# Performance work log

Hardware: AMD Instinct MI355X
Metric: run time of the kernel (lower is better)

Reference implementation:

```python
import jax, jax.numpy as jnp
import numpy as np

B, T_ENC, T_DEC = 1024, 96, 16
P_Q, CFG, H = 235, 32, 256
D_IN = P_Q + 5 + 10 + 3 + 3  # 256, matches input_size in __init__


def _lstm_step(x, h, c, Wih, Whh, bih, bhh):
    # torch.nn.LSTMCell: gate order i, f, g, o
    g = x @ Wih.T + bih + h @ Whh.T + bhh
    i, f, gg, o = jnp.split(g, 4, axis=-1)
    c2 = jax.nn.sigmoid(f) * c + jax.nn.sigmoid(i) * jnp.tanh(gg)
    h2 = jax.nn.sigmoid(o) * jnp.tanh(c2)
    return h2, c2


def setup_inputs():
    key = jax.random.key(0)
    ks = jax.random.split(key, 30)
    s = 0.05

    def n(i, shape):
        return jax.random.normal(ks[i], shape, jnp.float32) * s

    return {
        "input_p_q": jax.random.normal(ks[0], (B, T_ENC, P_Q), jnp.float32),
        "input_config": jax.random.normal(ks[1], (B, T_ENC, CFG), jnp.float32),
        "input_time": jax.random.randint(ks[2], (B, T_ENC, 3), 0, 5, jnp.int32),
        "W_cfg": n(3, (10, CFG)), "b_cfg": n(4, (10,)),
        "E_hour": n(5, (24, 5)), "E_wd": n(6, (8, 3)), "E_season": n(7, (5, 3)),
        "Wih_e": n(8, (4 * H, D_IN)), "Whh_e": n(9, (4 * H, H)),
        "bih_e": n(10, (4 * H,)), "bhh_e": n(11, (4 * H,)),
        "Wih_d": n(12, (4, H + 1)), "Whh_d": n(13, (4, 1)),
        "bih_d": n(14, (4,)), "bhh_d": n(15, (4,)),
        "Wi_s": n(16, (H, D_IN)), "bi_s": n(17, (H,)),
        "We_s": n(18, (H, 2 * H)),
        "Vd_s": n(19, (1, H)), "bVd_s": n(20, (1,)),
        "Wd_t": n(21, (H, H)), "bd_t": n(22, (H,)),
        "Wd2_t": n(23, (H, 2)),
        "Vd_t": n(24, (1, H)), "bVd_t": n(25, (1,)),
    }


def _forward(input_p_q, input_config, input_time, W_cfg, b_cfg, E_hour, E_wd, E_season,
             Wih_e, Whh_e, bih_e, bhh_e, Wih_d, Whh_d, bih_d, bhh_d,
             Wi_s, bi_s, We_s, Vd_s, bVd_s, Wd_t, bd_t, Wd2_t, Vd_t, bVd_t):
    b = input_p_q.shape[0]
    cfg = input_config @ W_cfg.T + b_cfg  # [B,T,10]
    inputs = jnp.concatenate([
        input_p_q, cfg,
        E_hour[input_time[:, :, 0]],
        E_wd[input_time[:, :, 1]],
        E_season[input_time[:, :, 2]],
    ], axis=2)  # [B,T,D_IN]

    # spatial_attention_Wi(inputs) hoisted out of the per-step loop (identical math)
    wi = inputs @ Wi_s.T + bi_s  # [B,T,H]

    def enc_step(carry, xt):
        hi, ci = carry
        x_t, wi_t = xt
        # Vd(tanh(We([h,c]) + Wi(x)))  -> [B,1] scalar gate (no softmax in original)
        a = jnp.tanh(jnp.concatenate([hi, ci], axis=1) @ We_s.T + wi_t) @ Vd_s.T + bVd_s
        h2, c2 = _lstm_step(x_t * a, hi, ci, Wih_e, Whh_e, bih_e, bhh_e)
        return (h2, c2), h2

    h0 = jnp.zeros((b, H), inputs.dtype)
    (_, _), mid = jax.lax.scan(enc_step, (h0, h0),
                               (inputs.transpose(1, 0, 2), wi.transpose(1, 0, 2)))
    mid = mid.transpose(1, 0, 2)  # [B,T,H]

    # temporal_attention_Wd(mid) does not depend on decode step -> hoisted
    wd_mid = mid @ Wd_t.T + bd_t  # [B,T,H]
    prev0 = mid[:, -1, 2:3]       # [B,1], as in original (element 2 of last hidden)

    def dec_step(carry, _):
        hi, ci, prev = carry
        q = jnp.concatenate([hi, ci], axis=1) @ Wd2_t.T       # [B,H]
        a = jnp.tanh(q[:, None, :] + wd_mid) @ Vd_t.T + bVd_t  # [B,T,1], raw scores
        ctx = jnp.einsum('bth,bt->bh', mid, a[..., 0])          # weighted sum over T
        h2, c2 = _lstm_step(jnp.concatenate([ctx, prev], axis=1), hi, ci,
                            Wih_d, Whh_d, bih_d, bhh_d)
        return (h2, c2, h2), h2

    z = jnp.zeros((b, 1), inputs.dtype)
    _, dec = jax.lax.scan(dec_step, (z, z, prev0), None, length=T_DEC)
    return dec.transpose(1, 0, 2)  # [B,16,1]


def reference(input_p_q, input_config, input_time, W_cfg, b_cfg, E_hour, E_wd, E_season,
              Wih_e, Whh_e, bih_e, bhh_e, Wih_d, Whh_d, bih_d, bhh_d,
              Wi_s, bi_s, We_s, Vd_s, bVd_s, Wd_t, bd_t, Wd2_t, Vd_t, bVd_t):
    return _forward(input_p_q, input_config, input_time, W_cfg, b_cfg, E_hour, E_wd,
                    E_season, Wih_e, Whh_e, bih_e, bhh_e, Wih_d, Whh_d, bih_d, bhh_d,
                    Wi_s, bi_s, We_s, Vd_s, bVd_s, Wd_t, bd_t, Wd2_t, Vd_t, bVd_t)
```

## Files before the change

### kernel.cpp

```cpp
#include <hip/hip_runtime.h>
#include <hip/hip_bf16.h>


typedef unsigned short ushort_t;
using short4v = __attribute__((ext_vector_type(4))) short;
using short8  = __attribute__((ext_vector_type(8))) short;
using floatx4 = __attribute__((ext_vector_type(4))) float;

#define DEVFN static __device__ __forceinline__

DEVFN float bs2f(ushort_t u) {
    union { float f; unsigned v; } c; c.v = ((unsigned)u) << 16; return c.f;
}
DEVFN ushort_t f2bs(float f) {
    __hip_bfloat16 h = __float2bfloat16(f);
    return *reinterpret_cast<ushort_t*>(&h);
}
DEVFN float gload(const void* p, long i, int bf) {
    if (bf) return bs2f(((const ushort_t*)p)[i]);
    return ((const float*)p)[i];
}
DEVFN float sigm(float x) { return 1.f / (1.f + __expf(-x)); }
DEVFN float ftanh(float x) {
    float t = __expf(-2.f * fabsf(x));
    float r = (1.f - t) / (1.f + t);
    return copysignf(r, x);
}
DEVFN short8 ld8(const ushort_t* p) { return *reinterpret_cast<const short8*>(p); }

DEVFN void bar_lgkm() {
    asm volatile("s_waitcnt lgkmcnt(0)" ::: "memory");
    __builtin_amdgcn_s_barrier();
}

#define GLD16R(dst, src) \
    asm volatile("global_load_dwordx4 %0, %1, off" : "+v"(dst) : "v"(src))

#define VW3() do { asm volatile("s_waitcnt vmcnt(3)"); \
                   __builtin_amdgcn_sched_barrier(0x3F7); } while (0)

struct SrcPtrs { const void* p[26]; };
struct WsPtrs {
    ushort_t *wcfg, *bcfg, *eh, *ew, *es, *wis, *bis, *wes, *vds, *bvds,
             *whh, *wih, *bih, *bhh, *wdt, *bdt, *wd2t, *vdt, *bvdt,
             *wihd, *whhd, *bihd, *bhhd;
};

__global__ void k_detect(const void* probe, int* flag) {
    if (threadIdx.x == 0 && blockIdx.x == 0) {
        const ushort_t* u = (const ushort_t*)probe;
        int ok = 1;
        for (int i = 0; i < 16; ++i) {
            ushort_t v = u[2 * i];
            int e = (v >> 7) & 0xFF;
            if (!(v == 0 || (e >= 96 && e <= 126))) ok = 0;
        }
        *flag = ok;
    }
}

__global__ __launch_bounds__(256) void k_cvt(SrcPtrs sp, WsPtrs wp, const int* flagp) {
    int bf = *flagp;
    const void* src = nullptr; ushort_t* dst = nullptr; long n = 0;
    switch (blockIdx.x) {
        case 0:  src = sp.p[3];  dst = wp.wcfg; n = 320;    break;
        case 1:  src = sp.p[4];  dst = wp.bcfg; n = 10;     break;
        case 2:  src = sp.p[5];  dst = wp.eh;   n = 120;    break;
        case 3:  src = sp.p[6];  dst = wp.ew;   n = 24;     break;
        case 4:  src = sp.p[7];  dst = wp.es;   n = 15;     break;
        case 5:  src = sp.p[16]; dst = wp.wis;  n = 65536;  break;
        case 6:  src = sp.p[17]; dst = wp.bis;  n = 256;    break;
        case 8:  src = sp.p[19]; dst = wp.vds;  n = 256;    break;
        case 9:  src = sp.p[20]; dst = wp.bvds; n = 1;      break;
        case 12: src = sp.p[10]; dst = wp.bih;  n = 1024;   break;
        case 13: src = sp.p[11]; dst = wp.bhh;  n = 1024;   break;
        case 14: src = sp.p[21]; dst = wp.wdt;  n = 65536;  break;
        case 15: src = sp.p[22]; dst = wp.bdt;  n = 256;    break;
        case 16: src = sp.p[23]; dst = wp.wd2t; n = 512;    break;
        case 17: src = sp.p[24]; dst = wp.vdt;  n = 256;    break;
        case 18: src = sp.p[25]; dst = wp.bvdt; n = 1;      break;
        case 19: src = sp.p[12]; dst = wp.wihd; n = 1028;   break;
        case 20: src = sp.p[13]; dst = wp.whhd; n = 4;      break;
        case 21: src = sp.p[14]; dst = wp.bihd; n = 4;      break;
        case 22: src = sp.p[15]; dst = wp.bhhd; n = 4;      break;
        default: return;
    }
    for (long i = threadIdx.x; i < n; i += 256) {
        float v = bf ? bs2f(((const ushort_t*)src)[i]) : ((const float*)src)[i];
        dst[i] = f2bs(v);
    }
}

__global__ __launch_bounds__(256) void k_permA(
    const void* whh_src, const void* wih_src,
    ushort_t* whhp, ushort_t* wihb, const int* flagp)
{
    int bf = *flagp;
    long base = (long)blockIdx.x * 2048;
    if (blockIdx.y == 1) {
#pragma unroll
        for (int ii = 0; ii < 8; ++ii) {
            long p = base + threadIdx.x + ii * 256;
            wihb[p] = f2bs(gload(wih_src, p, bf));
        }
        return;
    }
#pragma unroll
    for (int ii = 0; ii < 8; ++ii) {
        long p = base + threadIdx.x + ii * 256;
        int c = (int)(p >> 9), l = (int)((p >> 3) & 63), e = (int)(p & 7);
        int w = c >> 5, kk = (c >> 2) & 7, g = c & 3;
        int q = l >> 4, ln = l & 15;
        long si = (long)(g * 256 + w * 16 + ln) * 256 + kk * 32 + q * 8 + e;
        whhp[p] = f2bs(gload(whh_src, si, bf));
    }
}

__global__ __launch_bounds__(256) void k_permB(
    const void* wes_src, ushort_t* wesp, const int* flagp)
{
    int bf = *flagp;
    long base = (long)blockIdx.x * 2048;
#pragma unroll
    for (int ii = 0; ii < 8; ++ii) {
        long p = base + threadIdx.x + ii * 256;
        int c = (int)(p >> 9), l = (int)((p >> 3) & 63), e = (int)(p & 7);
        int w = c >> 4, kk = c & 15;
        int q = l >> 4, ln = l & 15;
        long si = (long)(w * 16 + ln) * 512 + kk * 32 + q * 8 + e;
        wesp[p] = f2bs(gload(wes_src, si, bf));
    }
}

__global__ __launch_bounds__(256) void k_build(
    const void* __restrict__ pq, const void* __restrict__ cfg_in,
    const int* __restrict__ timei, WsPtrs wp, const int* __restrict__ flagp,
    ushort_t* __restrict__ inputs)
{
    int bf = *flagp;
    int ch = threadIdx.x;
    for (int rr = 0; rr < 4; ++rr) {
        long row = (long)blockIdx.x * 4 + rr;
        float v;
        if (ch < 235) {
            v = gload(pq, row * 235 + ch, bf);
        } else if (ch < 245) {
            int j = ch - 235;
            float acc = bs2f(wp.bcfg[j]);
            for (int k = 0; k < 32; ++k)
                acc += gload(cfg_in, row * 32 + k, bf) * bs2f(wp.wcfg[j * 32 + k]);
            v = acc;
        } else if (ch < 250) {
            v = bs2f(wp.eh[timei[row * 3 + 0] * 5 + (ch - 245)]);
        } else if (ch < 253) {
            v = bs2f(wp.ew[timei[row * 3 + 1] * 3 + (ch - 250)]);
        } else {
            v = bs2f(wp.es[timei[row * 3 + 2] * 3 + (ch - 253)]);
        }
        inputs[row * 256 + ch] = f2bs(v);
    }
}

__global__ __launch_bounds__(256) void k_gemm(
    const ushort_t* __restrict__ A, const ushort_t* __restrict__ W,
    const ushort_t* __restrict__ bias, ushort_t* __restrict__ out,
    int ostride, int gatherB)
{
    const int K = 256;
    __shared__ alignas(16) ushort_t At[128][40];
    __shared__ alignas(16) ushort_t Bt[128][40];

    int tid  = threadIdx.x;
    int lane = tid & 63, wave = tid >> 6;
    int wm = wave >> 1, wn = wave & 1;
    int q = lane >> 4, ln = lane & 15;
    long mbase = (long)blockIdx.x * 128;

    floatx4 acc[4][4];
#pragma unroll
    for (int i = 0; i < 4; ++i)
#pragma unroll
        for (int j = 0; j < 4; ++j) acc[i][j] = (floatx4){0.f, 0.f, 0.f, 0.f};

    for (int k0 = 0; k0 < K; k0 += 32) {
        __syncthreads();
#pragma unroll
        for (int it = 0; it < 2; ++it) {
            int c = tid + it * 256;
            int r = c >> 2, kc = (c & 3) * 8;
            int wrow = gatherB ? (((r & 3) << 8) + ((int)blockIdx.y << 5) + (r >> 2))
                               : ((int)blockIdx.y * 128 + r);
            *reinterpret_cast<short8*>(&At[r][kc]) = ld8(&A[(mbase + r) * K + k0 + kc]);
            *reinterpret_cast<short8*>(&Bt[r][kc]) = ld8(&W[(long)wrow * K + k0 + kc]);
        }
        __syncthreads();
        short8 af[4];
#pragma unroll
        for (int mt = 0; mt < 4; ++mt)
            af[mt] = *reinterpret_cast<const short8*>(&At[wm * 64 + mt * 16 + ln][q * 8]);
#pragma unroll
        for (int nt = 0; nt < 4; ++nt) {
            short8 bf = *reinterpret_cast<const short8*>(&Bt[wn * 64 + nt * 16 + ln][q * 8]);
#pragma unroll
            for (int mt = 0; mt < 4; ++mt)
                acc[mt][nt] = __builtin_amdgcn_mfma_f32_16x16x32_bf16(af[mt], bf, acc[mt][nt], 0, 0, 0);
        }
    }

#pragma unroll
    for (int mt = 0; mt < 4; ++mt)
#pragma unroll
        for (int nt = 0; nt < 4; ++nt)
#pragma unroll
            for (int reg = 0; reg < 4; ++reg) {
                long row = mbase + wm * 64 + mt * 16 + q * 4 + reg;
                int  col = (int)blockIdx.y * 128 + wn * 64 + nt * 16 + ln;
                float bv = bias ? bs2f(bias[col]) : 0.f;
                out[row * (long)ostride + col] = f2bs(acc[mt][nt][reg] + bv);
            }
}

#define MFMA16(a, b, c) __builtin_amdgcn_mfma_f32_16x16x32_bf16((a), (b), (c), 0, 0, 0)

__global__ __launch_bounds__(512) void k_encoder(
    const ushort_t* __restrict__ wi, const ushort_t* __restrict__ ax,
    WsPtrs wp, ushort_t* __restrict__ mid)
{
    __shared__ alignas(16) ushort_t hcb[2][16][520];
    __shared__ alignas(16) float aPartT[16][20];
    __shared__ ushort_t occupancy_pad[30720];

    int tid  = threadIdx.x;
    int lane = tid & 63, w = tid >> 6;
    int q = lane >> 4, ln = lane & 15;
    long row0 = (long)blockIdx.x * 16;
    int u0 = w * 32 + ln;

    for (int i = tid; i < 2 * 16 * 520; i += 512) ((ushort_t*)hcb)[i] = 0;

    float bc[2][4], vds[2];
#pragma unroll
    for (int s = 0; s < 2; ++s) {
        int us = u0 + s * 16;
        bc[s][0] = bs2f(wp.bih[us])       + bs2f(wp.bhh[us]);
        bc[s][1] = bs2f(wp.bih[256 + us]) + bs2f(wp.bhh[256 + us]);
        bc[s][2] = bs2f(wp.bih[512 + us]) + bs2f(wp.bhh[512 + us]);
        bc[s][3] = bs2f(wp.bih[768 + us]) + bs2f(wp.bhh[768 + us]);
        vds[s]   = bs2f(wp.vds[us]);
    }
    float bVd = bs2f(wp.bvds[0]);

    const ushort_t* wesW0 = wp.wes + ((long)(2 * w)     << 13) + lane * 8;
    const ushort_t* wesW1 = wp.wes + ((long)(2 * w + 1) << 13) + lane * 8;
    const ushort_t* whhW0 = wp.whh + ((long)(2 * w)     << 14) + lane * 8;
    const ushort_t* whhW1 = wp.whh + ((long)(2 * w + 1) << 14) + lane * 8;

    const ushort_t* wiB0 = wi + ((row0 + q * 4) * 96) * 256 + u0;
    const ushort_t* axB0 = ax + ((row0 + q * 4) * 96) * 1024 + u0 * 4;

    int mr = tid >> 5, mc = (tid & 31) * 8;
    ushort_t* midB = mid + (row0 + mr) * 96 * 256 + mc;

    if (blockIdx.x > 60000) {
        occupancy_pad[tid] = (ushort_t)tid;
        midB[0] = occupancy_pad[(tid + 1) & 511];
    }

    float creg[2][4] = {{0.f, 0.f, 0.f, 0.f}, {0.f, 0.f, 0.f, 0.f}};
    __syncthreads();

    auto sp3 = [&](int j) -> const ushort_t* {
        if (j < 16)  return wesW0 + ((j & 15) << 9);
        if (j < 32)  return wesW1 + ((j & 15) << 9);
        if (j < 64)  return whhW0 + (((j - 32) & 31) << 9);
        return whhW1 + (((j - 64) & 31) << 9);
    };

    short8 Wr[4] = {};
#pragma unroll
    for (int j = 0; j < 4; ++j) GLD16R(Wr[j], sp3(j));

    for (int t = 0; t < 96; ++t) {
        ushort_t (*R)[520]  = hcb[t & 1];
        ushort_t (*Wb)[520] = hcb[(t & 1) ^ 1];

        {
            long toff = (long)(t > 0 ? t - 1 : 95) * 256;
            uint4 hv = *reinterpret_cast<const uint4*>(&R[mr][mc]);
            *reinterpret_cast<uint4*>(midB + toff) = hv;
        }
        short4v axv[2][4]; float wiv[2][4];
#pragma unroll
        for (int reg = 0; reg < 4; ++reg) {
            const ushort_t* a0 = axB0 + ((long)reg * 96 + t) * 1024;
            axv[0][reg] = *reinterpret_cast<const short4v*>(a0);
            axv[1][reg] = *reinterpret_cast<const short4v*>(a0 + 64);
            const ushort_t* w0 = wiB0 + ((long)reg * 96 + t) * 256;
            wiv[0][reg] = bs2f(w0[0]);
            wiv[1][reg] = bs2f(w0[16]);
        }

#pragma unroll
        for (int s = 0; s < 2; ++s) {
            floatx4 acc1 = (floatx4){0.f, 0.f, 0.f, 0.f};
#pragma unroll
            for (int c = 0; c < 16; ++c) {
                const int j = s * 16 + c;
                short8 af = ld8(&R[ln][c * 32 + q * 8]);
                VW3();
                acc1 = MFMA16(af, Wr[j & 3], acc1);
                GLD16R(Wr[j & 3], sp3((j + 4) % 96));
            }
            float p4[4];
#pragma unroll
            for (int reg = 0; reg < 4; ++reg)
                p4[reg] = ftanh(acc1[reg] + wiv[s][reg]) * vds[s];
#pragma unroll
            for (int m = 1; m < 16; m <<= 1) {
#pragma unroll
                for (int reg = 0; reg < 4; ++reg)
                    p4[reg] += __shfl_xor(p4[reg], m, 64);
            }
            if (ln == 0) {
                floatx4 pv = {p4[0], p4[1], p4[2], p4[3]};
                *reinterpret_cast<floatx4*>(&aPartT[2 * w + s][q * 4]) = pv;
            }
        }
        bar_lgkm();

        floatx4 av = {bVd, bVd, bVd, bVd};
#pragma unroll
        for (int ww = 0; ww < 16; ++ww)
            av += *reinterpret_cast<const floatx4*>(&aPartT[ww][q * 4]);

#pragma unroll
        for (int s = 0; s < 2; ++s) {
            floatx4 aH[4];
#pragma unroll
            for (int g = 0; g < 4; ++g) aH[g] = (floatx4){0.f, 0.f, 0.f, 0.f};
#pragma unroll
            for (int kk = 0; kk < 8; ++kk) {
                short8 af = ld8(&R[ln][kk * 32 + q * 8]);
#pragma unroll
                for (int g = 0; g < 4; ++g) {
                    const int j = 32 + s * 32 + kk * 4 + g;
                    VW3();
                    aH[g] = MFMA16(af, Wr[j & 3], aH[g]);
                    GLD16R(Wr[j & 3], sp3((j + 4) % 96));
                }
            }
            int us = u0 + s * 16;
#pragma unroll
            for (int reg = 0; reg < 4; ++reg) {
                float a  = av[reg];
                float gi = aH[0][reg] + a * bs2f((ushort_t)axv[s][reg][0]) + bc[s][0];
                float gf = aH[1][reg] + a * bs2f((ushort_t)axv[s][reg][1]) + bc[s][1];
                float gg = aH[2][reg] + a * bs2f((ushort_t)axv[s][reg][2]) + bc[s][2];
                float go = aH[3][reg] + a * bs2f((ushort_t)axv[s][reg][3]) + bc[s][3];
                float c2 = sigm(gf) * creg[s][reg] + sigm(gi) * ftanh(gg);
                float h2 = sigm(go) * ftanh(c2);
                creg[s][reg] = c2;
                int r = q * 4 + reg;
                Wb[r][us] = f2bs(h2);
                Wb[r][256 + us] = f2bs(c2);
            }
        }
        bar_lgkm();
    }

    asm volatile("s_waitcnt vmcnt(0)" ::: "memory");
    {
        uint4 hv = *reinterpret_cast<const uint4*>(&hcb[0][mr][mc]);
        *reinterpret_cast<uint4*>(midB + 95L * 256) = hv;
    }
}

__global__ __launch_bounds__(256) void k_decoder(
    const ushort_t* __restrict__ mid, const ushort_t* __restrict__ wd,
    WsPtrs wp, const int* __restrict__ flagp, void* __restrict__ out)
{
    __shared__ ushort_t wdl[96][264];
    __shared__ float qL[256], aLs[96], ctxL[256], VdtL[256], gL[4];
    __shared__ float st[3];

    int tid = threadIdx.x;
    long b = blockIdx.x;
    int bf = *flagp;

    for (int c = tid; c < 96 * 256; c += 256) {
        int tp = c >> 8, chn = c & 255;
        wdl[tp][chn] = wd[(b * 96 + tp) * 256 + chn];
    }
    qL[tid] = 0.f; ctxL[tid] = 0.f;
    if (tid < 96) aLs[tid] = 0.f;
    if (tid < 4)  gL[tid] = 0.f;
    VdtL[tid] = bs2f(wp.vdt[tid]);
    if (tid == 0) {
        st[0] = 0.f; st[1] = 0.f;
        st[2] = bs2f(mid[(b * 96 + 95) * 256 + 2]);
    }
    float bVdt = bs2f(wp.bvdt[0]);
    float w2a = bs2f(wp.wd2t[tid * 2]), w2b = bs2f(wp.wd2t[tid * 2 + 1]);
    __syncthreads();

    for (int s = 0; s < 16; ++s) {
        float hi = st[0], ci = st[1], prev = st[2];
        qL[tid] = hi * w2a + ci * w2b;
        __syncthreads();
        {
            int v = tid >> 6, l = tid & 63;
            for (int tp = v; tp < 96; tp += 4) {
                float sacc = 0.f;
#pragma unroll
                for (int e = 0; e < 4; ++e) {
                    int u = l * 4 + e;
                    sacc += ftanh(qL[u] + bs2f(wdl[tp][u])) * VdtL[u];
                }
#pragma unroll
                for (int m = 1; m < 64; m <<= 1) sacc += __shfl_xor(sacc, m, 64);
                if (l == 0) aLs[tp] = sacc + bVdt;
            }
        }
        __syncthreads();
        {
            float acc = 0.f;
            for (int tp = 0; tp < 96; ++tp)
                acc += aLs[tp] * bs2f(mid[(b * 96 + tp) * 256 + tid]);
            ctxL[tid] = acc;
        }
        __syncthreads();
        {
            int g = tid >> 6, k = tid & 63;
            float part = 0.f;
#pragma unroll
            for (int e = 0; e < 4; ++e) {
                int u = k + e * 64;
                part += bs2f(wp.wihd[g * 257 + u]) * ctxL[u];
            }
#pragma unroll
            for (int m = 1; m < 64; m <<= 1) part += __shfl_xor(part, m, 64);
            if (k == 0)
                gL[g] = part + bs2f(wp.bihd[g]) + bs2f(wp.bhhd[g])
                      + bs2f(wp.whhd[g]) * hi + bs2f(wp.wihd[g * 257 + 256]) * prev;
        }
        __syncthreads();
        if (tid == 0) {
            float c2 = sigm(gL[1]) * ci + sigm(gL[0]) * ftanh(gL[2]);
            float h2 = sigm(gL[3]) * ftanh(c2);
            st[0] = h2; st[1] = c2; st[2] = h2;
            long oi = b * 16 + s;
            if (bf) ((ushort_t*)out)[oi] = f2bs(h2);
            else    ((float*)out)[oi] = h2;
        }
        __syncthreads();
    }
}

extern "C" void kernel_launch(void* const* d_in, const int* in_sizes, int n_in,
                              void* d_out, int out_size, void* d_ws, size_t ws_size,
                              hipStream_t stream)
{
    const long MT = 1024L * 96;

    int* flagp = (int*)d_ws;
    ushort_t* base = (ushort_t*)((char*)d_ws + 256);

    SrcPtrs sp;
    for (int i = 0; i < 26; ++i) sp.p[i] = d_in[i];

    static const long sizes[23] = {
        320, 10, 120, 24, 15, 65536, 256, 131072, 256, 1,
        262144, 262144, 1024, 1024, 65536, 256, 512, 256, 1,
        1028, 4, 4, 4
    };
    ushort_t* ptrs[23];
    long off = 0;
    for (int i = 0; i < 23; ++i) {
        ptrs[i] = base + off;
        off += (sizes[i] + 7) & ~7L;
    }

    WsPtrs wp;
    wp.wcfg = ptrs[0];  wp.bcfg = ptrs[1];  wp.eh   = ptrs[2];  wp.ew   = ptrs[3];
    wp.es   = ptrs[4];  wp.wis  = ptrs[5];  wp.bis  = ptrs[6];  wp.wes  = ptrs[7];
    wp.vds  = ptrs[8];  wp.bvds = ptrs[9];  wp.whh  = ptrs[10]; wp.wih  = ptrs[11];
    wp.bih  = ptrs[12]; wp.bhh  = ptrs[13]; wp.wdt  = ptrs[14]; wp.bdt  = ptrs[15];
    wp.wd2t = ptrs[16]; wp.vdt  = ptrs[17]; wp.bvdt = ptrs[18]; wp.wihd = ptrs[19];
    wp.whhd = ptrs[20]; wp.bihd = ptrs[21]; wp.bhhd = ptrs[22];

    ushort_t* inputs = base + off;
    ushort_t* wib    = inputs + MT * 256;
    ushort_t* midb   = wib + MT * 256;
    ushort_t* axb    = midb + MT * 256;
    ushort_t* wdb    = wib;

    k_detect<<<1, 64, 0, stream>>>(d_in[3], flagp);
    k_cvt<<<23, 256, 0, stream>>>(sp, wp, flagp);
    k_permA<<<dim3(128, 2), 256, 0, stream>>>(d_in[9], d_in[8], wp.whh, wp.wih, flagp);
    k_permB<<<64, 256, 0, stream>>>(d_in[18], wp.wes, flagp);
    k_build<<<24576, 256, 0, stream>>>(d_in[0], d_in[1], (const int*)d_in[2],
                                       wp, flagp, inputs);
    k_gemm<<<dim3(768, 2), 256, 0, stream>>>(inputs, wp.wis, wp.bis, wib, 256, 0);
    k_gemm<<<dim3(768, 8), 256, 0, stream>>>(inputs, wp.wih, nullptr, axb, 1024, 1);
    k_encoder<<<64, 512, 0, stream>>>(wib, axb, wp, midb);
    k_gemm<<<dim3(768, 2), 256, 0, stream>>>(midb, wp.wdt, wp.bdt, wdb, 256, 0);
    k_decoder<<<1024, 256, 0, stream>>>(midb, wdb, wp, flagp, d_out);
}
```

Baseline: 2.287 ms.

## Deepen weight prefetch ring to 8 and interleave both sub-tiles per A-fragment

```diff
diff --git a/kernel.cpp b/kernel.cpp
--- a/kernel.cpp
+++ b/kernel.cpp
@@ -36,7 +36,7 @@
 #define GLD16R(dst, src) \
     asm volatile("global_load_dwordx4 %0, %1, off" : "+v"(dst) : "v"(src))
 
-#define VW3() do { asm volatile("s_waitcnt vmcnt(3)"); \
+#define VW7() do { asm volatile("s_waitcnt vmcnt(7)"); \
                    __builtin_amdgcn_sched_barrier(0x3F7); } while (0)
 
 struct SrcPtrs { const void* p[26]; };
@@ -270,15 +270,17 @@
     __syncthreads();
 
     auto sp3 = [&](int j) -> const ushort_t* {
-        if (j < 16)  return wesW0 + ((j & 15) << 9);
-        if (j < 32)  return wesW1 + ((j & 15) << 9);
-        if (j < 64)  return whhW0 + (((j - 32) & 31) << 9);
-        return whhW1 + (((j - 64) & 31) << 9);
+        if (j < 32) {
+            int s = j & 1, c = j >> 1;
+            return (s ? wesW1 : wesW0) + (c << 9);
+        }
+        int jj = j - 32, s = jj & 1, c = jj >> 1;
+        return (s ? whhW1 : whhW0) + (c << 9);
     };
 
-    short8 Wr[4] = {};
-#pragma unroll
-    for (int j = 0; j < 4; ++j) GLD16R(Wr[j], sp3(j));
+    short8 Wr[8] = {};
+#pragma unroll
+    for (int j = 0; j < 8; ++j) GLD16R(Wr[j], sp3(j));
 
     for (int t = 0; t < 96; ++t) {
         ushort_t (*R)[520]  = hcb[t & 1];
@@ -300,29 +302,39 @@
             wiv[1][reg] = bs2f(w0[16]);
         }
 
-#pragma unroll
-        for (int s = 0; s < 2; ++s) {
-            floatx4 acc1 = (floatx4){0.f, 0.f, 0.f, 0.f};
-#pragma unroll
-            for (int c = 0; c < 16; ++c) {
-                const int j = s * 16 + c;
-                short8 af = ld8(&R[ln][c * 32 + q * 8]);
-                VW3();
-                acc1 = MFMA16(af, Wr[j & 3], acc1);
-                GLD16R(Wr[j & 3], sp3((j + 4) % 96));
-            }
-            float p4[4];
+        floatx4 acc1[2];
+        acc1[0] = (floatx4){0.f, 0.f, 0.f, 0.f};
+        acc1[1] = (floatx4){0.f, 0.f, 0.f, 0.f};
+#pragma unroll
+        for (int c = 0; c < 16; ++c) {
+            short8 af = ld8(&R[ln][c * 32 + q * 8]);
+#pragma unroll
+            for (int s = 0; s < 2; ++s) {
+                const int j = c * 2 + s;
+                VW7();
+                acc1[s] = MFMA16(af, Wr[j & 7], acc1[s]);
+                GLD16R(Wr[j & 7], sp3((j + 8) % 96));
+            }
+        }
+
+        float p4[2][4];
+#pragma unroll
+        for (int s = 0; s < 2; ++s)
 #pragma unroll
             for (int reg = 0; reg < 4; ++reg)
-                p4[reg] = ftanh(acc1[reg] + wiv[s][reg]) * vds[s];
-#pragma unroll
-            for (int m = 1; m < 16; m <<= 1) {
+                p4[s][reg] = ftanh(acc1[s][reg] + wiv[s][reg]) * vds[s];
+#pragma unroll
+        for (int m = 1; m < 16; m <<= 1) {
+#pragma unroll
+            for (int s = 0; s < 2; ++s)
 #pragma unroll
                 for (int reg = 0; reg < 4; ++reg)
-                    p4[reg] += __shfl_xor(p4[reg], m, 64);
-            }
-            if (ln == 0) {
-                floatx4 pv = {p4[0], p4[1], p4[2], p4[3]};
+                    p4[s][reg] += __shfl_xor(p4[s][reg], m, 64);
+        }
+        if (ln == 0) {
+#pragma unroll
+            for (int s = 0; s < 2; ++s) {
+                floatx4 pv = {p4[s][0], p4[s][1], p4[s][2], p4[s][3]};
                 *reinterpret_cast<floatx4*>(&aPartT[2 * w + s][q * 4]) = pv;
             }
         }
@@ -333,30 +345,36 @@
         for (int ww = 0; ww < 16; ++ww)
             av += *reinterpret_cast<const floatx4*>(&aPartT[ww][q * 4]);
 
+        floatx4 aH[2][4];
+#pragma unroll
+        for (int s = 0; s < 2; ++s)
+#pragma unroll
+            for (int g = 0; g < 4; ++g) aH[s][g] = (floatx4){0.f, 0.f, 0.f, 0.f};
+#pragma unroll
+        for (int kk = 0; kk < 8; ++kk) {
+            short8 af = ld8(&R[ln][kk * 32 + q * 8]);
+#pragma unroll
+            for (int g = 0; g < 4; ++g) {
+#pragma unroll
+                for (int s = 0; s < 2; ++s) {
+                    const int j = 32 + (kk * 4 + g) * 2 + s;
+                    VW7();
+                    aH[s][g] = MFMA16(af, Wr[j & 7], aH[s][g]);
+                    GLD16R(Wr[j & 7], sp3((j + 8) % 96));
+                }
+            }
+        }
+
 #pragma unroll
         for (int s = 0; s < 2; ++s) {
-            floatx4 aH[4];
-#pragma unroll
-            for (int g = 0; g < 4; ++g) aH[g] = (floatx4){0.f, 0.f, 0.f, 0.f};
-#pragma unroll
-            for (int kk = 0; kk < 8; ++kk) {
-                short8 af = ld8(&R[ln][kk * 32 + q * 8]);
-#pragma unroll
-                for (int g = 0; g < 4; ++g) {
-                    const int j = 32 + s * 32 + kk * 4 + g;
-                    VW3();
-                    aH[g] = MFMA16(af, Wr[j & 3], aH[g]);
-                    GLD16R(Wr[j & 3], sp3((j + 4) % 96));
-                }
-            }
             int us = u0 + s * 16;
 #pragma unroll
             for (int reg = 0; reg < 4; ++reg) {
                 float a  = av[reg];
-                float gi = aH[0][reg] + a * bs2f((ushort_t)axv[s][reg][0]) + bc[s][0];
-                float gf = aH[1][reg] + a * bs2f((ushort_t)axv[s][reg][1]) + bc[s][1];
-                float gg = aH[2][reg] + a * bs2f((ushort_t)axv[s][reg][2]) + bc[s][2];
-                float go = aH[3][reg] + a * bs2f((ushort_t)axv[s][reg][3]) + bc[s][3];
+                float gi = aH[s][0][reg] + a * bs2f((ushort_t)axv[s][reg][0]) + bc[s][0];
+                float gf = aH[s][1][reg] + a * bs2f((ushort_t)axv[s][reg][1]) + bc[s][1];
+                float gg = aH[s][2][reg] + a * bs2f((ushort_t)axv[s][reg][2]) + bc[s][2];
+                float go = aH[s][3][reg] + a * bs2f((ushort_t)axv[s][reg][3]) + bc[s][3];
                 float c2 = sigm(gf) * creg[s][reg] + sigm(gi) * ftanh(gg);
                 float h2 = sigm(go) * ftanh(c2);
                 creg[s][reg] = c2;
```

After: 2.831 ms. +23.8%, slower.

## Fuse input projections into one GEMM with A tile resident in LDS

Applied to the files above, without the earlier changes.

```diff
diff --git a/kernel.cpp b/kernel.cpp
--- a/kernel.cpp
+++ b/kernel.cpp
@@ -161,13 +161,15 @@
     }
 }
 
-__global__ __launch_bounds__(256) void k_gemm(
-    const ushort_t* __restrict__ A, const ushort_t* __restrict__ W,
-    const ushort_t* __restrict__ bias, ushort_t* __restrict__ out,
-    int ostride, int gatherB)
-{
-    const int K = 256;
-    __shared__ alignas(16) ushort_t At[128][40];
+#define MFMA16(a, b, c) __builtin_amdgcn_mfma_f32_16x16x32_bf16((a), (b), (c), 0, 0, 0)
+
+__global__ __launch_bounds__(256) void k_gemmN(
+    const ushort_t* __restrict__ A, const ushort_t* __restrict__ Wg,
+    const ushort_t* __restrict__ Ws, const ushort_t* __restrict__ bias,
+    ushort_t* __restrict__ outg, ushort_t* __restrict__ outs,
+    int nax, int ns)
+{
+    __shared__ alignas(16) ushort_t At[128][264];
     __shared__ alignas(16) ushort_t Bt[128][40];
 
     int tid  = threadIdx.x;
@@ -176,51 +178,72 @@
     int q = lane >> 4, ln = lane & 15;
     long mbase = (long)blockIdx.x * 128;
 
-    floatx4 acc[4][4];
-#pragma unroll
-    for (int i = 0; i < 4; ++i)
-#pragma unroll
-        for (int j = 0; j < 4; ++j) acc[i][j] = (floatx4){0.f, 0.f, 0.f, 0.f};
-
-    for (int k0 = 0; k0 < K; k0 += 32) {
-        __syncthreads();
-#pragma unroll
-        for (int it = 0; it < 2; ++it) {
-            int c = tid + it * 256;
-            int r = c >> 2, kc = (c & 3) * 8;
-            int wrow = gatherB ? (((r & 3) << 8) + ((int)blockIdx.y << 5) + (r >> 2))
-                               : ((int)blockIdx.y * 128 + r);
-            *reinterpret_cast<short8*>(&At[r][kc]) = ld8(&A[(mbase + r) * K + k0 + kc]);
-            *reinterpret_cast<short8*>(&Bt[r][kc]) = ld8(&W[(long)wrow * K + k0 + kc]);
-        }
-        __syncthreads();
-        short8 af[4];
+#pragma unroll
+    for (int it = 0; it < 16; ++it) {
+        int idx = tid + it * 256;
+        int r = idx >> 5, u = idx & 31;
+        *reinterpret_cast<short8*>(&At[r][u * 8]) =
+            ld8(&A[(mbase + r) * 256 + u * 8]);
+    }
+    __syncthreads();
+
+    const int ny = nax + ns;
+    for (int y = 0; y < ny; ++y) {
+        floatx4 acc[4][4];
+#pragma unroll
+        for (int i = 0; i < 4; ++i)
+#pragma unroll
+            for (int j = 0; j < 4; ++j) acc[i][j] = (floatx4){0.f, 0.f, 0.f, 0.f};
+
+        for (int k0 = 0; k0 < 256; k0 += 32) {
+            __syncthreads();
+#pragma unroll
+            for (int it = 0; it < 2; ++it) {
+                int c = tid + it * 256;
+                int r = c >> 2, kc = (c & 3) * 8;
+                const ushort_t* src;
+                if (y < nax) {
+                    int wrow = ((r & 3) << 8) + (y << 5) + (r >> 2);
+                    src = &Wg[(long)wrow * 256 + k0 + kc];
+                } else {
+                    int wrow = ((y - nax) << 7) + r;
+                    src = &Ws[(long)wrow * 256 + k0 + kc];
+                }
+                *reinterpret_cast<short8*>(&Bt[r][kc]) = ld8(src);
+            }
+            __syncthreads();
+            short8 af[4];
+#pragma unroll
+            for (int mt = 0; mt < 4; ++mt)
+                af[mt] = ld8(&At[wm * 64 + mt * 16 + ln][k0 + q * 8]);
+#pragma unroll
+            for (int nt = 0; nt < 4; ++nt) {
+                short8 bf = ld8(&Bt[wn * 64 + nt * 16 + ln][q * 8]);
+#pragma unroll
+                for (int mt = 0; mt < 4; ++mt)
+                    acc[mt][nt] = MFMA16(af[mt], bf, acc[mt][nt]);
+            }
+        }
+
 #pragma unroll
         for (int mt = 0; mt < 4; ++mt)
-            af[mt] = *reinterpret_cast<const short8*>(&At[wm * 64 + mt * 16 + ln][q * 8]);
-#pragma unroll
-        for (int nt = 0; nt < 4; ++nt) {
-            short8 bf = *reinterpret_cast<const short8*>(&Bt[wn * 64 + nt * 16 + ln][q * 8]);
-#pragma unroll
-            for (int mt = 0; mt < 4; ++mt)
-                acc[mt][nt] = __builtin_amdgcn_mfma_f32_16x16x32_bf16(af[mt], bf, acc[mt][nt], 0, 0, 0);
-        }
-    }
-
-#pragma unroll
-    for (int mt = 0; mt < 4; ++mt)
-#pragma unroll
-        for (int nt = 0; nt < 4; ++nt)
-#pragma unroll
-            for (int reg = 0; reg < 4; ++reg) {
-                long row = mbase + wm * 64 + mt * 16 + q * 4 + reg;
-                int  col = (int)blockIdx.y * 128 + wn * 64 + nt * 16 + ln;
-                float bv = bias ? bs2f(bias[col]) : 0.f;
-                out[row * (long)ostride + col] = f2bs(acc[mt][nt][reg] + bv);
-            }
-}
-
-#define MFMA16(a, b, c) __builtin_amdgcn_mfma_f32_16x16x32_bf16((a), (b), (c), 0, 0, 0)
+#pragma unroll
+            for (int nt = 0; nt < 4; ++nt)
+#pragma unroll
+                for (int reg = 0; reg < 4; ++reg) {
+                    long row = mbase + wm * 64 + mt * 16 + q * 4 + reg;
+                    int  cc  = wn * 64 + nt * 16 + ln;
+                    if (y < nax) {
+                        int col = (y << 7) + cc;
+                        outg[row * 1024L + col] = f2bs(acc[mt][nt][reg]);
+                    } else {
+                        int col = ((y - nax) << 7) + cc;
+                        outs[row * 256L + col] =
+                            f2bs(acc[mt][nt][reg] + bs2f(bias[col]));
+                    }
+                }
+    }
+}
 
 __global__ __launch_bounds__(512) void k_encoder(
     const ushort_t* __restrict__ wi, const ushort_t* __restrict__ ax,
@@ -500,9 +523,10 @@
     k_permB<<<64, 256, 0, stream>>>(d_in[18], wp.wes, flagp);
     k_build<<<24576, 256, 0, stream>>>(d_in[0], d_in[1], (const int*)d_in[2],
                                        wp, flagp, inputs);
-    k_gemm<<<dim3(768, 2), 256, 0, stream>>>(inputs, wp.wis, wp.bis, wib, 256, 0);
-    k_gemm<<<dim3(768, 8), 256, 0, stream>>>(inputs, wp.wih, nullptr, axb, 1024, 1);
+    k_gemmN<<<768, 256, 0, stream>>>(inputs, wp.wih, wp.wis, wp.bis,
+                                     axb, wib, 8, 2);
     k_encoder<<<64, 512, 0, stream>>>(wib, axb, wp, midb);
-    k_gemm<<<dim3(768, 2), 256, 0, stream>>>(midb, wp.wdt, wp.bdt, wdb, 256, 0);
+    k_gemmN<<<768, 256, 0, stream>>>(midb, nullptr, wp.wdt, wp.bdt,
+                                     nullptr, wdb, 0, 2);
     k_decoder<<<1024, 256, 0, stream>>>(midb, wdb, wp, flagp, d_out);
 }
```

Result: no change. 2.306 ms (+0.8%).
